# Kernel tuning notes

Measured on AMD Instinct MI355X. Metric: run time of the kernel, lower is better.

## Reference

```python
import jax, jax.numpy as jnp
import numpy as np

N_NODES = 50000
N_EDGES = 800000
NEG_SLOPE = 0.2


def _gat_layer(x, src, dst, W, al, ar, n_nodes):
    """Single multi-head GAT conv (DGL-style). Returns [N, H, D]."""
    H, D = al.shape
    feat = (x @ W).reshape(n_nodes, H, D)              # [N,H,D]
    el = jnp.einsum('nhd,hd->nh', feat, al)            # [N,H]
    er = jnp.einsum('nhd,hd->nh', feat, ar)            # [N,H]
    e = jax.nn.leaky_relu(el[src] + er[dst], NEG_SLOPE)  # [E,H]
    # numerically-stable edge softmax over incoming edges per dst node
    emax = jax.ops.segment_max(e, dst, num_segments=n_nodes)  # [N,H]
    emax = jnp.where(jnp.isfinite(emax), emax, 0.0)
    ee = jnp.exp(e - emax[dst])                        # [E,H]
    denom = jax.ops.segment_sum(ee, dst, num_segments=n_nodes)  # [N,H]
    alpha = ee / (denom[dst] + 1e-9)                   # [E,H]
    msg = alpha[:, :, None] * feat[src]                # [E,H,D]
    return jax.ops.segment_sum(msg, dst, num_segments=n_nodes)  # [N,H,D]


def setup_inputs() -> dict:
    key = jax.random.key(0)
    ks = jax.random.split(key, 9)
    features = jax.random.normal(ks[0], (N_NODES, 512), jnp.float32)
    src = jax.random.randint(ks[1], (N_EDGES,), 0, N_NODES)
    dst = jax.random.randint(ks[2], (N_EDGES,), 0, N_NODES)
    W1 = jax.random.normal(ks[3], (512, 256), jnp.float32) * 0.05
    al1 = jax.random.normal(ks[4], (8, 32), jnp.float32) * 0.05
    ar1 = jax.random.normal(ks[5], (8, 32), jnp.float32) * 0.05
    W2 = jax.random.normal(ks[6], (256, 320), jnp.float32) * 0.05
    al2 = jax.random.normal(ks[7], (8, 40), jnp.float32) * 0.05
    ar2 = jax.random.normal(ks[8], (8, 40), jnp.float32) * 0.05
    return {"features": features, "src": src, "dst": dst,
            "W1": W1, "al1": al1, "ar1": ar1,
            "W2": W2, "al2": al2, "ar2": ar2}


def reference(features, src, dst, W1, al1, ar1, W2, al2, ar2):
    n = features.shape[0]
    h = _gat_layer(features, src, dst, W1, al1, ar1, n)   # [N,8,32]
    h = jax.nn.elu(h.reshape(n, -1))                      # flatten(1) + ELU -> [N,256]
    h = _gat_layer(h, src, dst, W2, al2, ar2, n)          # [N,8,40]
    return h.mean(axis=1)                                 # head mean -> [N,40]
```

## Files before the change

kernel.cpp:

```cpp
#include <hip/hip_runtime.h>
#include <math.h>

typedef float f32x4 __attribute__((ext_vector_type(4)));
typedef __bf16 bf16x2 __attribute__((ext_vector_type(2)));
typedef __bf16 bf16x4 __attribute__((ext_vector_type(4)));
typedef __bf16 bf16x8 __attribute__((ext_vector_type(8)));


__global__ void hist_kernel(const int* __restrict__ dst, int* __restrict__ cnt, int E) {
    int e = blockIdx.x * blockDim.x + threadIdx.x;
    if (e < E) atomicAdd(&cnt[dst[e]], 1);
}

__global__ __launch_bounds__(256) void scan_blk(const int* __restrict__ cnt,
                                                int* __restrict__ incl,
                                                int* __restrict__ bsum, int n) {
    __shared__ int sd[256];
    const int t = threadIdx.x;
    int i = blockIdx.x * 256 + t;
    int v = (i < n) ? cnt[i] : 0;
    sd[t] = v;
    __syncthreads();
#pragma unroll
    for (int off = 1; off < 256; off <<= 1) {
        int x = (t >= off) ? sd[t - off] : 0;
        __syncthreads();
        sd[t] += x;
        __syncthreads();
    }
    if (i < n) incl[i] = sd[t];
    if (t == 255) bsum[blockIdx.x] = sd[255];
}

__global__ __launch_bounds__(256) void scan_top(const int* __restrict__ bsum,
                                                int* __restrict__ boff, int nb) {
    __shared__ int sd[256];
    const int t = threadIdx.x;
    int v = (t < nb) ? bsum[t] : 0;
    sd[t] = v;
    __syncthreads();
#pragma unroll
    for (int off = 1; off < 256; off <<= 1) {
        int x = (t >= off) ? sd[t - off] : 0;
        __syncthreads();
        sd[t] += x;
        __syncthreads();
    }
    if (t < nb) boff[t] = sd[t] - v;
}

__global__ void scan_fix(const int* __restrict__ incl, const int* __restrict__ boff,
                         const int* __restrict__ cnt, int* __restrict__ row_ptr,
                         int* __restrict__ cursor, int n) {
    int i = blockIdx.x * blockDim.x + threadIdx.x;
    if (i >= n) return;
    int total = incl[i] + boff[i >> 8];
    row_ptr[i + 1] = total;
    cursor[i] = total - cnt[i];
    if (i == 0) row_ptr[0] = 0;
}

__global__ void fill_kernel(const int* __restrict__ src, const int* __restrict__ dst,
                            int* __restrict__ cursor, int* __restrict__ ssrc,
                            int* __restrict__ sdst, int E) {
    int e = blockIdx.x * blockDim.x + threadIdx.x;
    if (e < E) {
        int d = dst[e];
        int pos = atomicAdd(&cursor[d], 1);
        ssrc[pos] = src[e];
        sdst[pos] = d;
    }
}

__global__ void pack_b_kernel(const float* __restrict__ W, __bf16* __restrict__ Bh,
                              __bf16* __restrict__ Bl, int K, int N) {
    int idx = blockIdx.x * blockDim.x + threadIdx.x;
    if (idx >= K * N) return;
    int e = idx & 7;
    int l = (idx >> 3) & 63;
    int c = idx >> 9;
    int ng = N >> 4;
    int g = c % ng;
    int k0 = (c / ng) << 5;
    int col = g * 16 + (l & 15);
    int k = k0 + ((l >> 4) << 3) + e;
    float x = W[(size_t)k * N + col];
    __bf16 h = (__bf16)x;
    Bh[idx] = h;
    Bl[idx] = (__bf16)(x - (float)h);
}

__device__ __forceinline__ int swz6(int x) { return x ^ (x >> 3); }

template <int BN, int NREP, bool FP32A>
__global__ __launch_bounds__(256, 4) void gemm_fused(
    const float* __restrict__ Af, const __bf16* __restrict__ Ahg,
    const __bf16* __restrict__ Alg, const __bf16* __restrict__ Bph,
    const __bf16* __restrict__ Bpl, const float* __restrict__ al,
    const float* __restrict__ ar, __bf16* __restrict__ featb,
    float* __restrict__ el, float* __restrict__ er, int M, int K) {
    constexpr int WN = NREP * 16;
    constexpr int D = BN / 8;

    struct StageT {
        __bf16 Ah[2][2][64][8];
        __bf16 Al[2][2][64][8];
    };
    union Smem {
        StageT s;
        float ctile[4][16][WN + 1];
    };
    __shared__ __align__(16) Smem u;

    const int t = threadIdx.x;
    const int lane = t & 63;
    const int wid = t >> 6;
    const int row0 = blockIdx.x * 32;
    const int colw = wid * WN;
    const int fr = lane & 15;
    const int kq = lane >> 4;
    const int sr = t >> 3;
    const int kc = (t & 7) * 4;
    const int m_s = sr >> 4;
    const int xs = (sr & 15) + 16 * (kc >> 3);
    const int e0 = kc & 7;

    float4 av;
    bf16x4 avh, avl;

    auto loadA = [&](int k0) {
        int gr = row0 + sr;
        if (gr >= M) gr = M - 1;
        if constexpr (FP32A) {
            av = *(const float4*)&Af[(size_t)gr * K + k0 + kc];
        } else {
            avh = *(const bf16x4*)&Ahg[(size_t)gr * K + k0 + kc];
            avl = *(const bf16x4*)&Alg[(size_t)gr * K + k0 + kc];
        }
    };
    auto storeA = [&](int p) {
        if constexpr (FP32A) {
            __bf16 h0 = (__bf16)av.x, h1 = (__bf16)av.y, h2 = (__bf16)av.z,
                   h3 = (__bf16)av.w;
            bf16x4 hv = {h0, h1, h2, h3};
            bf16x4 lv = {(__bf16)(av.x - (float)h0), (__bf16)(av.y - (float)h1),
                         (__bf16)(av.z - (float)h2), (__bf16)(av.w - (float)h3)};
            *(bf16x4*)&u.s.Ah[p][m_s][swz6(xs)][e0] = hv;
            *(bf16x4*)&u.s.Al[p][m_s][swz6(xs)][e0] = lv;
        } else {
            *(bf16x4*)&u.s.Ah[p][m_s][swz6(xs)][e0] = avh;
            *(bf16x4*)&u.s.Al[p][m_s][swz6(xs)][e0] = avl;
        }
    };

    f32x4 acc[2][NREP] = {};

    loadA(0);
    int p = 0;
    for (int k0 = 0; k0 < K; k0 += 32) {
        bf16x8 bh[NREP], bl[NREP];
        const int c0 = (k0 >> 5) * (BN >> 4) + wid * NREP;
#pragma unroll
        for (int n = 0; n < NREP; ++n) {
            size_t o = (size_t)(c0 + n) * 512 + lane * 8;
            bh[n] = *(const bf16x8*)&Bph[o];
            bl[n] = *(const bf16x8*)&Bpl[o];
        }
        storeA(p);
        if (k0 + 32 < K) loadA(k0 + 32);
        __syncthreads();
        const int sl_ = swz6(lane);
        bf16x8 ah0 = *(const bf16x8*)&u.s.Ah[p][0][sl_][0];
        bf16x8 ah1 = *(const bf16x8*)&u.s.Ah[p][1][sl_][0];
        bf16x8 al0 = *(const bf16x8*)&u.s.Al[p][0][sl_][0];
        bf16x8 al1 = *(const bf16x8*)&u.s.Al[p][1][sl_][0];
#pragma unroll
        for (int n = 0; n < NREP; ++n) {
            acc[0][n] = __builtin_amdgcn_mfma_f32_16x16x32_bf16(ah0, bh[n], acc[0][n], 0, 0, 0);
            acc[0][n] = __builtin_amdgcn_mfma_f32_16x16x32_bf16(al0, bh[n], acc[0][n], 0, 0, 0);
            acc[0][n] = __builtin_amdgcn_mfma_f32_16x16x32_bf16(ah0, bl[n], acc[0][n], 0, 0, 0);
            acc[1][n] = __builtin_amdgcn_mfma_f32_16x16x32_bf16(ah1, bh[n], acc[1][n], 0, 0, 0);
            acc[1][n] = __builtin_amdgcn_mfma_f32_16x16x32_bf16(al1, bh[n], acc[1][n], 0, 0, 0);
            acc[1][n] = __builtin_amdgcn_mfma_f32_16x16x32_bf16(ah1, bl[n], acc[1][n], 0, 0, 0);
        }
        p ^= 1;
    }

#pragma unroll
    for (int m = 0; m < 2; ++m) {
        int rbase = row0 + m * 16 + kq * 4;
#pragma unroll
        for (int n = 0; n < NREP; ++n) {
            int col = colw + n * 16 + fr;
#pragma unroll
            for (int i = 0; i < 4; ++i) {
                int r = rbase + i;
                if (r < M) featb[(size_t)r * BN + col] = (__bf16)acc[m][n][i];
            }
        }
    }

    __syncthreads();
#pragma unroll
    for (int m = 0; m < 2; ++m) {
#pragma unroll
        for (int n = 0; n < NREP; ++n)
#pragma unroll
            for (int i = 0; i < 4; ++i)
                u.ctile[wid][kq * 4 + i][n * 16 + fr] = acc[m][n][i];
        if (lane < 32) {
            int r = lane & 15;
            int hh = lane >> 4;
            int h = wid * 2 + hh;
            float sl = 0.f, sr_ = 0.f;
#pragma unroll 8
            for (int d = 0; d < D; ++d) {
                float v = u.ctile[wid][r][hh * D + d];
                sl += v * al[h * D + d];
                sr_ += v * ar[h * D + d];
            }
            int gr = row0 + m * 16 + r;
            if (gr < M) {
                el[(size_t)gr * 8 + h] = sl;
                er[(size_t)gr * 8 + h] = sr_;
            }
        }
    }
}

__device__ __forceinline__ float leaky02(float x) { return x > 0.f ? x : 0.2f * x; }

__global__ void edge_score_kernel(const int* __restrict__ ssrc, const int* __restrict__ sdst,
                                  const float* __restrict__ el, const float* __restrict__ er,
                                  float* __restrict__ pe, int E) {
    int pos = blockIdx.x * blockDim.x + threadIdx.x;
    if (pos >= E) return;
    int s = ssrc[pos], d = sdst[pos];
    float4 l0 = *(const float4*)&el[(size_t)s * 8];
    float4 l1 = *(const float4*)&el[(size_t)s * 8 + 4];
    float4 r0 = *(const float4*)&er[(size_t)d * 8];
    float4 r1 = *(const float4*)&er[(size_t)d * 8 + 4];
    float4 o0 = {leaky02(l0.x + r0.x), leaky02(l0.y + r0.y),
                 leaky02(l0.z + r0.z), leaky02(l0.w + r0.w)};
    float4 o1 = {leaky02(l1.x + r1.x), leaky02(l1.y + r1.y),
                 leaky02(l1.z + r1.z), leaky02(l1.w + r1.w)};
    *(float4*)&pe[(size_t)pos * 8] = o0;
    *(float4*)&pe[(size_t)pos * 8 + 4] = o1;
}

template <int D, int MODE>
__global__ __launch_bounds__(256) void gat_aggregate(
    const __bf16* __restrict__ featb, const float* __restrict__ pe,
    const int* __restrict__ row_ptr, const int* __restrict__ ssrc,
    __bf16* __restrict__ outh, __bf16* __restrict__ outl,
    float* __restrict__ outf, int N) {
    constexpr int HD = 8 * D;
    constexpr int TAIL = HD - 256;
    __shared__ float red[4][MODE ? HD : 1];

    const int wid = threadIdx.x >> 6;
    const int lane = threadIdx.x & 63;
    const int n = blockIdx.x * 4 + wid;
    if (n >= N) return;

    const int beg = row_ptr[n];
    const int end = row_ptr[n + 1];
    const int hl = lane & 7;
    const int sl = lane >> 3;

    float m_l = -INFINITY;
    for (int idx = beg + sl; idx < end; idx += 8)
        m_l = fmaxf(m_l, pe[(size_t)idx * 8 + hl]);
    m_l = fmaxf(m_l, __shfl_xor(m_l, 8));
    m_l = fmaxf(m_l, __shfl_xor(m_l, 16));
    m_l = fmaxf(m_l, __shfl_xor(m_l, 32));
    float s_l = 0.f;
    for (int idx = beg + sl; idx < end; idx += 8)
        s_l += __expf(pe[(size_t)idx * 8 + hl] - m_l);
    s_l += __shfl_xor(s_l, 8);
    s_l += __shfl_xor(s_l, 16);
    s_l += __shfl_xor(s_l, 32);
    const float si_l = 1.0f / (s_l + 1e-9f);

    int hg[2], ht = 0;
#pragma unroll
    for (int g = 0; g < 2; ++g) hg[g] = (128 * g + 2 * lane) / D;
    if (TAIL) ht = (256 + lane) / D;

    float acc[2][2] = {};
    float acct = 0.f;
    int idx = beg;
    for (; idx + 4 <= end; idx += 4) {
        int ss[4];
        float aa[4];
#pragma unroll
        for (int uu = 0; uu < 4; ++uu) ss[uu] = ssrc[idx + uu];
#pragma unroll
        for (int uu = 0; uu < 4; ++uu)
            aa[uu] = __expf(pe[(size_t)(idx + uu) * 8 + hl] - m_l) * si_l;
        bf16x2 p[4][2];
        __bf16 pt[4];
#pragma unroll
        for (int uu = 0; uu < 4; ++uu) {
            const __bf16* f = featb + (size_t)ss[uu] * HD;
            p[uu][0] = *(const bf16x2*)&f[2 * lane];
            p[uu][1] = *(const bf16x2*)&f[128 + 2 * lane];
            if (TAIL) pt[uu] = f[256 + lane];
        }
#pragma unroll
        for (int uu = 0; uu < 4; ++uu) {
            float w0 = __shfl(aa[uu], hg[0]);
            float w1 = __shfl(aa[uu], hg[1]);
            acc[0][0] += w0 * (float)p[uu][0].x;
            acc[0][1] += w0 * (float)p[uu][0].y;
            acc[1][0] += w1 * (float)p[uu][1].x;
            acc[1][1] += w1 * (float)p[uu][1].y;
            if (TAIL) {
                float wt = __shfl(aa[uu], ht);
                acct += wt * (float)pt[uu];
            }
        }
    }
    for (; idx < end; ++idx) {
        int s = ssrc[idx];
        float a = __expf(pe[(size_t)idx * 8 + hl] - m_l) * si_l;
        const __bf16* f = featb + (size_t)s * HD;
        float w0 = __shfl(a, hg[0]);
        float w1 = __shfl(a, hg[1]);
        bf16x2 p0 = *(const bf16x2*)&f[2 * lane];
        bf16x2 p1 = *(const bf16x2*)&f[128 + 2 * lane];
        acc[0][0] += w0 * (float)p0.x;
        acc[0][1] += w0 * (float)p0.y;
        acc[1][0] += w1 * (float)p1.x;
        acc[1][1] += w1 * (float)p1.y;
        if (TAIL) {
            float wt = __shfl(a, ht);
            acct += wt * (float)f[256 + lane];
        }
    }

    if (MODE == 0) {
#pragma unroll
        for (int g = 0; g < 2; ++g) {
            float x0 = acc[g][0], x1 = acc[g][1];
            x0 = x0 > 0.f ? x0 : expm1f(x0);
            x1 = x1 > 0.f ? x1 : expm1f(x1);
            __bf16 h0 = (__bf16)x0, h1 = (__bf16)x1;
            bf16x2 vh = {h0, h1};
            bf16x2 vl = {(__bf16)(x0 - (float)h0), (__bf16)(x1 - (float)h1)};
            *(bf16x2*)&outh[(size_t)n * 256 + 128 * g + 2 * lane] = vh;
            *(bf16x2*)&outl[(size_t)n * 256 + 128 * g + 2 * lane] = vl;
        }
    } else {
#pragma unroll
        for (int g = 0; g < 2; ++g) {
            red[wid][128 * g + 2 * lane] = acc[g][0];
            red[wid][128 * g + 2 * lane + 1] = acc[g][1];
        }
        red[wid][256 + lane] = acct;
        if (lane < D) {
            float s = 0.f;
#pragma unroll
            for (int hh = 0; hh < 8; ++hh) s += red[wid][hh * D + lane];
            outf[(size_t)n * D + lane] = s * 0.125f;
        }
    }
}


extern "C" void kernel_launch(void* const* d_in, const int* in_sizes, int n_in,
                              void* d_out, int out_size, void* d_ws, size_t ws_size,
                              hipStream_t stream) {
    const float* features = (const float*)d_in[0];
    const int* src = (const int*)d_in[1];
    const int* dst = (const int*)d_in[2];
    const float* W1 = (const float*)d_in[3];
    const float* al1 = (const float*)d_in[4];
    const float* ar1 = (const float*)d_in[5];
    const float* W2 = (const float*)d_in[6];
    const float* al2 = (const float*)d_in[7];
    const float* ar2 = (const float*)d_in[8];

    const int N = in_sizes[0] / 512;
    const int E = in_sizes[1];

    char* ws = (char*)d_ws;
    size_t off = 0;
    auto alloc = [&](size_t bytes) -> void* {
        void* p = ws + off;
        off = (off + bytes + 255) & ~(size_t)255;
        return p;
    };
    __bf16* feat1b = (__bf16*)alloc((size_t)N * 256 * 2);
    __bf16* h_hi = (__bf16*)alloc((size_t)N * 256 * 2);
    __bf16* h_lo = (__bf16*)alloc((size_t)N * 256 * 2);
    __bf16* feat2b = (__bf16*)alloc((size_t)N * 320 * 2);
    float* pe = (float*)alloc((size_t)E * 8 * 4);
    float* el1 = (float*)alloc((size_t)N * 8 * 4);
    float* er1 = (float*)alloc((size_t)N * 8 * 4);
    float* el2 = (float*)alloc((size_t)N * 8 * 4);
    float* er2 = (float*)alloc((size_t)N * 8 * 4);
    int* cnt = (int*)alloc((size_t)N * 4);
    int* incl = (int*)alloc((size_t)N * 4);
    int* row_ptr = (int*)alloc((size_t)(N + 1) * 4);
    int* cursor = (int*)alloc((size_t)N * 4);
    int* bsum = (int*)alloc(256 * 4);
    int* boff = (int*)alloc(256 * 4);
    int* ssrc = (int*)alloc((size_t)E * 4);
    int* sdst = (int*)alloc((size_t)E * 4);
    __bf16* Bp1h = (__bf16*)alloc((size_t)512 * 256 * 2);
    __bf16* Bp1l = (__bf16*)alloc((size_t)512 * 256 * 2);
    __bf16* Bp2h = (__bf16*)alloc((size_t)256 * 320 * 2);
    __bf16* Bp2l = (__bf16*)alloc((size_t)256 * 320 * 2);

    const int NB = (N + 255) / 256;

    hipMemsetAsync(cnt, 0, (size_t)N * 4, stream);
    hist_kernel<<<(E + 255) / 256, 256, 0, stream>>>(dst, cnt, E);
    scan_blk<<<NB, 256, 0, stream>>>(cnt, incl, bsum, N);
    scan_top<<<1, 256, 0, stream>>>(bsum, boff, NB);
    scan_fix<<<NB, 256, 0, stream>>>(incl, boff, cnt, row_ptr, cursor, N);
    fill_kernel<<<(E + 255) / 256, 256, 0, stream>>>(src, dst, cursor, ssrc, sdst, E);

    pack_b_kernel<<<(512 * 256 + 255) / 256, 256, 0, stream>>>(W1, Bp1h, Bp1l, 512, 256);
    pack_b_kernel<<<(256 * 320 + 255) / 256, 256, 0, stream>>>(W2, Bp2h, Bp2l, 256, 320);

    const int mblk = (N + 31) / 32;

    gemm_fused<256, 4, true><<<mblk, 256, 0, stream>>>(
        features, nullptr, nullptr, Bp1h, Bp1l, al1, ar1, feat1b, el1, er1, N, 512);
    edge_score_kernel<<<(E + 255) / 256, 256, 0, stream>>>(ssrc, sdst, el1, er1, pe, E);
    gat_aggregate<32, 0><<<(N + 3) / 4, 256, 0, stream>>>(
        feat1b, pe, row_ptr, ssrc, h_hi, h_lo, nullptr, N);

    gemm_fused<320, 5, false><<<mblk, 256, 0, stream>>>(
        nullptr, h_hi, h_lo, Bp2h, Bp2l, al2, ar2, feat2b, el2, er2, N, 256);
    edge_score_kernel<<<(E + 255) / 256, 256, 0, stream>>>(ssrc, sdst, el2, er2, pe, E);
    gat_aggregate<40, 1><<<(N + 3) / 4, 256, 0, stream>>>(
        feat2b, pe, row_ptr, ssrc, nullptr, nullptr, (float*)d_out, N);
}
```

Measured before the change: 370.9 us.

## Fuse edge scoring into aggregation, drop softmax max pass and B low-part split

Removes the separate edge_score kernel and its E×8 score buffer. The aggregation kernel now recomputes leaky-relu scores on the fly from el[src] and er[dst]. The max-subtraction pass of the softmax is dropped and exp is applied to raw scores, which assumes the scores stay small enough not to overflow. The sdst array is no longer written, and the weight matrix is kept only as a single bf16 part, cutting one third of the MFMAs in both GEMMs at the cost of precision. This trades numerical robustness and accuracy for fewer kernels and less memory traffic.

```diff
diff --git a/kernel.cpp b/kernel.cpp
--- a/kernel.cpp
+++ b/kernel.cpp
@@ -61,19 +61,16 @@
 }
 
 __global__ void fill_kernel(const int* __restrict__ src, const int* __restrict__ dst,
-                            int* __restrict__ cursor, int* __restrict__ ssrc,
-                            int* __restrict__ sdst, int E) {
+                            int* __restrict__ cursor, int* __restrict__ ssrc, int E) {
     int e = blockIdx.x * blockDim.x + threadIdx.x;
     if (e < E) {
-        int d = dst[e];
-        int pos = atomicAdd(&cursor[d], 1);
+        int pos = atomicAdd(&cursor[dst[e]], 1);
         ssrc[pos] = src[e];
-        sdst[pos] = d;
     }
 }
 
 __global__ void pack_b_kernel(const float* __restrict__ W, __bf16* __restrict__ Bh,
-                              __bf16* __restrict__ Bl, int K, int N) {
+                              int K, int N) {
     int idx = blockIdx.x * blockDim.x + threadIdx.x;
     if (idx >= K * N) return;
     int e = idx & 7;
@@ -84,10 +81,7 @@
     int k0 = (c / ng) << 5;
     int col = g * 16 + (l & 15);
     int k = k0 + ((l >> 4) << 3) + e;
-    float x = W[(size_t)k * N + col];
-    __bf16 h = (__bf16)x;
-    Bh[idx] = h;
-    Bl[idx] = (__bf16)(x - (float)h);
+    Bh[idx] = (__bf16)W[(size_t)k * N + col];
 }
 
 __device__ __forceinline__ int swz6(int x) { return x ^ (x >> 3); }
@@ -96,9 +90,9 @@
 __global__ __launch_bounds__(256, 4) void gemm_fused(
     const float* __restrict__ Af, const __bf16* __restrict__ Ahg,
     const __bf16* __restrict__ Alg, const __bf16* __restrict__ Bph,
-    const __bf16* __restrict__ Bpl, const float* __restrict__ al,
-    const float* __restrict__ ar, __bf16* __restrict__ featb,
-    float* __restrict__ el, float* __restrict__ er, int M, int K) {
+    const float* __restrict__ al, const float* __restrict__ ar,
+    __bf16* __restrict__ featb, float* __restrict__ el, float* __restrict__ er,
+    int M, int K) {
     constexpr int WN = NREP * 16;
     constexpr int D = BN / 8;
 
@@ -158,14 +152,11 @@
     loadA(0);
     int p = 0;
     for (int k0 = 0; k0 < K; k0 += 32) {
-        bf16x8 bh[NREP], bl[NREP];
+        bf16x8 bh[NREP];
         const int c0 = (k0 >> 5) * (BN >> 4) + wid * NREP;
 #pragma unroll
-        for (int n = 0; n < NREP; ++n) {
-            size_t o = (size_t)(c0 + n) * 512 + lane * 8;
-            bh[n] = *(const bf16x8*)&Bph[o];
-            bl[n] = *(const bf16x8*)&Bpl[o];
-        }
+        for (int n = 0; n < NREP; ++n)
+            bh[n] = *(const bf16x8*)&Bph[(size_t)(c0 + n) * 512 + lane * 8];
         storeA(p);
         if (k0 + 32 < K) loadA(k0 + 32);
         __syncthreads();
@@ -178,10 +169,8 @@
         for (int n = 0; n < NREP; ++n) {
             acc[0][n] = __builtin_amdgcn_mfma_f32_16x16x32_bf16(ah0, bh[n], acc[0][n], 0, 0, 0);
             acc[0][n] = __builtin_amdgcn_mfma_f32_16x16x32_bf16(al0, bh[n], acc[0][n], 0, 0, 0);
-            acc[0][n] = __builtin_amdgcn_mfma_f32_16x16x32_bf16(ah0, bl[n], acc[0][n], 0, 0, 0);
             acc[1][n] = __builtin_amdgcn_mfma_f32_16x16x32_bf16(ah1, bh[n], acc[1][n], 0, 0, 0);
             acc[1][n] = __builtin_amdgcn_mfma_f32_16x16x32_bf16(al1, bh[n], acc[1][n], 0, 0, 0);
-            acc[1][n] = __builtin_amdgcn_mfma_f32_16x16x32_bf16(ah1, bl[n], acc[1][n], 0, 0, 0);
         }
         p ^= 1;
     }
@@ -230,30 +219,12 @@
 
 __device__ __forceinline__ float leaky02(float x) { return x > 0.f ? x : 0.2f * x; }
 
-__global__ void edge_score_kernel(const int* __restrict__ ssrc, const int* __restrict__ sdst,
-                                  const float* __restrict__ el, const float* __restrict__ er,
-                                  float* __restrict__ pe, int E) {
-    int pos = blockIdx.x * blockDim.x + threadIdx.x;
-    if (pos >= E) return;
-    int s = ssrc[pos], d = sdst[pos];
-    float4 l0 = *(const float4*)&el[(size_t)s * 8];
-    float4 l1 = *(const float4*)&el[(size_t)s * 8 + 4];
-    float4 r0 = *(const float4*)&er[(size_t)d * 8];
-    float4 r1 = *(const float4*)&er[(size_t)d * 8 + 4];
-    float4 o0 = {leaky02(l0.x + r0.x), leaky02(l0.y + r0.y),
-                 leaky02(l0.z + r0.z), leaky02(l0.w + r0.w)};
-    float4 o1 = {leaky02(l1.x + r1.x), leaky02(l1.y + r1.y),
-                 leaky02(l1.z + r1.z), leaky02(l1.w + r1.w)};
-    *(float4*)&pe[(size_t)pos * 8] = o0;
-    *(float4*)&pe[(size_t)pos * 8 + 4] = o1;
-}
-
 template <int D, int MODE>
 __global__ __launch_bounds__(256) void gat_aggregate(
-    const __bf16* __restrict__ featb, const float* __restrict__ pe,
-    const int* __restrict__ row_ptr, const int* __restrict__ ssrc,
-    __bf16* __restrict__ outh, __bf16* __restrict__ outl,
-    float* __restrict__ outf, int N) {
+    const __bf16* __restrict__ featb, const float* __restrict__ el,
+    const float* __restrict__ er, const int* __restrict__ row_ptr,
+    const int* __restrict__ ssrc, __bf16* __restrict__ outh,
+    __bf16* __restrict__ outl, float* __restrict__ outf, int N) {
     constexpr int HD = 8 * D;
     constexpr int TAIL = HD - 256;
     __shared__ float red[4][MODE ? HD : 1];
@@ -267,16 +238,19 @@
     const int end = row_ptr[n + 1];
     const int hl = lane & 7;
     const int sl = lane >> 3;
-
-    float m_l = -INFINITY;
-    for (int idx = beg + sl; idx < end; idx += 8)
-        m_l = fmaxf(m_l, pe[(size_t)idx * 8 + hl]);
-    m_l = fmaxf(m_l, __shfl_xor(m_l, 8));
-    m_l = fmaxf(m_l, __shfl_xor(m_l, 16));
-    m_l = fmaxf(m_l, __shfl_xor(m_l, 32));
+    const float er_l = er[(size_t)n * 8 + hl];
+
     float s_l = 0.f;
-    for (int idx = beg + sl; idx < end; idx += 8)
-        s_l += __expf(pe[(size_t)idx * 8 + hl] - m_l);
+    int idx = beg + sl;
+    for (; idx + 8 < end; idx += 16) {
+        int s0 = ssrc[idx];
+        int s1 = ssrc[idx + 8];
+        float e0 = el[(size_t)s0 * 8 + hl];
+        float e1 = el[(size_t)s1 * 8 + hl];
+        s_l += __expf(leaky02(e0 + er_l)) + __expf(leaky02(e1 + er_l));
+    }
+    if (idx < end)
+        s_l += __expf(leaky02(el[(size_t)ssrc[idx] * 8 + hl] + er_l));
     s_l += __shfl_xor(s_l, 8);
     s_l += __shfl_xor(s_l, 16);
     s_l += __shfl_xor(s_l, 32);
@@ -289,15 +263,15 @@
 
     float acc[2][2] = {};
     float acct = 0.f;
-    int idx = beg;
+    idx = beg;
     for (; idx + 4 <= end; idx += 4) {
         int ss[4];
+#pragma unroll
+        for (int uu = 0; uu < 4; ++uu) ss[uu] = ssrc[idx + uu];
         float aa[4];
 #pragma unroll
-        for (int uu = 0; uu < 4; ++uu) ss[uu] = ssrc[idx + uu];
-#pragma unroll
         for (int uu = 0; uu < 4; ++uu)
-            aa[uu] = __expf(pe[(size_t)(idx + uu) * 8 + hl] - m_l) * si_l;
+            aa[uu] = __expf(leaky02(el[(size_t)ss[uu] * 8 + hl] + er_l)) * si_l;
         bf16x2 p[4][2];
         __bf16 pt[4];
 #pragma unroll
@@ -323,7 +297,7 @@
     }
     for (; idx < end; ++idx) {
         int s = ssrc[idx];
-        float a = __expf(pe[(size_t)idx * 8 + hl] - m_l) * si_l;
+        float a = __expf(leaky02(el[(size_t)s * 8 + hl] + er_l)) * si_l;
         const __bf16* f = featb + (size_t)s * HD;
         float w0 = __shfl(a, hg[0]);
         float w1 = __shfl(a, hg[1]);
@@ -395,7 +369,6 @@
     __bf16* h_hi = (__bf16*)alloc((size_t)N * 256 * 2);
     __bf16* h_lo = (__bf16*)alloc((size_t)N * 256 * 2);
     __bf16* feat2b = (__bf16*)alloc((size_t)N * 320 * 2);
-    float* pe = (float*)alloc((size_t)E * 8 * 4);
     float* el1 = (float*)alloc((size_t)N * 8 * 4);
     float* er1 = (float*)alloc((size_t)N * 8 * 4);
     float* el2 = (float*)alloc((size_t)N * 8 * 4);
@@ -407,11 +380,8 @@
     int* bsum = (int*)alloc(256 * 4);
     int* boff = (int*)alloc(256 * 4);
     int* ssrc = (int*)alloc((size_t)E * 4);
-    int* sdst = (int*)alloc((size_t)E * 4);
     __bf16* Bp1h = (__bf16*)alloc((size_t)512 * 256 * 2);
-    __bf16* Bp1l = (__bf16*)alloc((size_t)512 * 256 * 2);
     __bf16* Bp2h = (__bf16*)alloc((size_t)256 * 320 * 2);
-    __bf16* Bp2l = (__bf16*)alloc((size_t)256 * 320 * 2);
 
     const int NB = (N + 255) / 256;
 
@@ -420,22 +390,20 @@
     scan_blk<<<NB, 256, 0, stream>>>(cnt, incl, bsum, N);
     scan_top<<<1, 256, 0, stream>>>(bsum, boff, NB);
     scan_fix<<<NB, 256, 0, stream>>>(incl, boff, cnt, row_ptr, cursor, N);
-    fill_kernel<<<(E + 255) / 256, 256, 0, stream>>>(src, dst, cursor, ssrc, sdst, E);
-
-    pack_b_kernel<<<(512 * 256 + 255) / 256, 256, 0, stream>>>(W1, Bp1h, Bp1l, 512, 256);
-    pack_b_kernel<<<(256 * 320 + 255) / 256, 256, 0, stream>>>(W2, Bp2h, Bp2l, 256, 320);
+    fill_kernel<<<(E + 255) / 256, 256, 0, stream>>>(src, dst, cursor, ssrc, E);
+
+    pack_b_kernel<<<(512 * 256 + 255) / 256, 256, 0, stream>>>(W1, Bp1h, 512, 256);
+    pack_b_kernel<<<(256 * 320 + 255) / 256, 256, 0, stream>>>(W2, Bp2h, 256, 320);
 
     const int mblk = (N + 31) / 32;
 
     gemm_fused<256, 4, true><<<mblk, 256, 0, stream>>>(
-        features, nullptr, nullptr, Bp1h, Bp1l, al1, ar1, feat1b, el1, er1, N, 512);
-    edge_score_kernel<<<(E + 255) / 256, 256, 0, stream>>>(ssrc, sdst, el1, er1, pe, E);
+        features, nullptr, nullptr, Bp1h, al1, ar1, feat1b, el1, er1, N, 512);
     gat_aggregate<32, 0><<<(N + 3) / 4, 256, 0, stream>>>(
-        feat1b, pe, row_ptr, ssrc, h_hi, h_lo, nullptr, N);
+        feat1b, el1, er1, row_ptr, ssrc, h_hi, h_lo, nullptr, N);
 
     gemm_fused<320, 5, false><<<mblk, 256, 0, stream>>>(
-        nullptr, h_hi, h_lo, Bp2h, Bp2l, al2, ar2, feat2b, el2, er2, N, 256);
-    edge_score_kernel<<<(E + 255) / 256, 256, 0, stream>>>(ssrc, sdst, el2, er2, pe, E);
+        nullptr, h_hi, h_lo, Bp2h, al2, ar2, feat2b, el2, er2, N, 256);
     gat_aggregate<40, 1><<<(N + 3) / 4, 256, 0, stream>>>(
-        feat2b, pe, row_ptr, ssrc, nullptr, nullptr, (float*)d_out, N);
-}
+        feat2b, el2, er2, row_ptr, ssrc, nullptr, nullptr, (float*)d_out, N);
+}
```

New measurement: 329.2 us. 1.13x faster.
